# Performance work log

Hardware: AMD Instinct MI355X
Metric: run time of the kernel (lower is better)

Reference implementation:

```python
import jax, jax.numpy as jnp
import numpy as np

N_NODES = 100000
N_EDGES = 1600000
IN_F, HID, OUT_F = 256, 128, 48
ALPHA = 0.01
K = 10
# SparseDropout with dropout_prob=0 keeps all edges but scales by 1/(1-0+1e-5)
DROP_SCALE = 1.0 / (1.0 + 1e-5)


def setup_inputs() -> dict:
    key = jax.random.key(0)
    ks = jax.random.split(key, 8)
    x = jax.random.normal(ks[0], (N_NODES, IN_F), dtype=jnp.float32)
    rows = jax.random.randint(ks[1], (N_EDGES,), 0, N_NODES, dtype=jnp.int32)
    cols = jax.random.randint(ks[2], (N_EDGES,), 0, N_NODES, dtype=jnp.int32)
    vals = jax.random.uniform(ks[3], (N_EDGES,), dtype=jnp.float32)
    # Linear params (Kaiming-uniform-ish like torch defaults)
    lim1 = 1.0 / np.sqrt(IN_F)
    W1 = jax.random.uniform(ks[4], (IN_F, HID), minval=-lim1, maxval=lim1, dtype=jnp.float32)
    b1 = jax.random.uniform(ks[5], (HID,), minval=-lim1, maxval=lim1, dtype=jnp.float32)
    lim2 = 1.0 / np.sqrt(HID)
    W2 = jax.random.uniform(ks[6], (HID, OUT_F), minval=-lim2, maxval=lim2, dtype=jnp.float32)
    b2 = jax.random.uniform(ks[7], (OUT_F,), minval=-lim2, maxval=lim2, dtype=jnp.float32)
    return {"x": x, "rows": rows, "cols": cols, "vals": vals,
            "W1": W1, "b1": b1, "W2": W2, "b2": b2}


def reference(x, rows, cols, vals, W1, b1, W2, b2):
    # MLP (dropout=0 -> identity)
    h = jax.nn.relu(x @ W1 + b1)          # [N, HID]
    h = h @ W2 + b2                        # [N, OUT_F]
    v = vals * DROP_SCALE                  # SparseDropout(p=0) value scaling
    # K-step APPNP propagation: h <- (1-alpha) * A @ h + alpha * h
    def step(h, _):
        ah = jax.ops.segment_sum(v[:, None] * h[cols], rows, num_segments=N_NODES)
        return (1.0 - ALPHA) * ah + ALPHA * h, None
    h, _ = jax.lax.scan(step, h, None, length=K)
    return h
```

## Files before the change

kernel.cpp:

```cpp
#include <hip/hip_runtime.h>

#define N_NODES 100000
#define N_EDGES 1600000
#define IN_F 256
#define HID 128
#define OUT_F 48
#define PAD_F 64
#define ALPHA 0.01f
#define K_STEPS 10
#define DROP_SCALE (1.0f / (1.0f + 1e-5f))

#define NBUCK 196
#define BCAP 10240
#define EPB 4096
#define ROW_MASK_CLR 0xFFFFFFFFFC01FFFFULL

#define MLP_BLOCKS ((N_NODES / 16 + 3) / 4)
#define BUCKET_BLOCKS ((N_EDGES + EPB - 1) / EPB)

typedef __bf16 v8bf __attribute__((ext_vector_type(8)));
typedef float v4f __attribute__((ext_vector_type(4)));
typedef unsigned long long u64;

static __device__ __forceinline__ __bf16 tobf(float f) { return (__bf16)f; }

__global__ __launch_bounds__(256) void conv_w(const float* __restrict__ W1,
                                              const float* __restrict__ W2,
                                              __bf16* __restrict__ w1t,
                                              __bf16* __restrict__ w2t) {
  int i = blockIdx.x * 256 + threadIdx.x;
  if (i < HID * IN_F) {
    int n = i >> 8, k = i & 255;
    w1t[i] = tobf(W1[k * HID + n]);
  }
  int j = i - HID * IN_F;
  if (j >= 0 && j < OUT_F * HID) {
    int n = j >> 7, k = j & 127;
    w2t[j] = tobf(W2[k * OUT_F + n]);
  }
}

__global__ __launch_bounds__(256, 4) void fused_mlp_bucket(
    const float* __restrict__ x, const __bf16* __restrict__ w1t,
    const float* __restrict__ b1, const __bf16* __restrict__ w2t,
    const float* __restrict__ b2, __bf16* __restrict__ h0,
    const int* __restrict__ rows, const int* __restrict__ cols,
    const float* __restrict__ vals, int* __restrict__ bcur,
    u64* __restrict__ brec) {
  __shared__ __bf16 h1s[64][136];
  __shared__ int lhist[NBUCK];
  __shared__ int lbase[NBUCK];

  const int tid = threadIdx.x;

  if (blockIdx.x < MLP_BLOCKS) {
    const int wv = tid >> 6;
    const int l = tid & 63;
    const int lm = l & 15;
    const int ko = (l >> 4) * 8;
    const int gw = blockIdx.x * 4 + wv;
    if (gw >= N_NODES / 16) return;
    const int n0w = gw * 16;
    const int xrow = n0w + lm;

    const float* xb = x + (size_t)xrow * IN_F + ko;
    float4 xr[16];
#pragma unroll
    for (int k0 = 0; k0 < 8; k0++) {
      xr[2 * k0] = *(const float4*)(xb + k0 * 32);
      xr[2 * k0 + 1] = *(const float4*)(xb + k0 * 32 + 4);
    }

    v4f acc1[8];
#pragma unroll
    for (int nf = 0; nf < 8; nf++) acc1[nf] = (v4f){0.f, 0.f, 0.f, 0.f};

#pragma unroll
    for (int k0 = 0; k0 < 8; k0++) {
      const float* f0 = (const float*)&xr[2 * k0];
      v8bf a;
#pragma unroll
      for (int j = 0; j < 8; j++) a[j] = tobf(f0[j]);
      const __bf16* w1base = w1t + (size_t)lm * IN_F + k0 * 32 + ko;
#pragma unroll
      for (int nf = 0; nf < 8; nf++) {
        v8bf b = *(const v8bf*)(w1base + nf * 16 * IN_F);
        acc1[nf] = __builtin_amdgcn_mfma_f32_16x16x32_bf16(a, b, acc1[nf], 0, 0, 0);
      }
    }

#pragma unroll
    for (int nf = 0; nf < 8; nf++) {
      float bb = b1[nf * 16 + lm];
#pragma unroll
      for (int q = 0; q < 4; q++) {
        int rr = (wv << 4) + (l >> 4) * 4 + q;
        h1s[rr][nf * 16 + lm] = tobf(fmaxf(acc1[nf][q] + bb, 0.f));
      }
    }
    __syncthreads();

    const int lrow = (wv << 4) + lm;
    v4f acc2[3];
#pragma unroll
    for (int nf = 0; nf < 3; nf++) acc2[nf] = (v4f){0.f, 0.f, 0.f, 0.f};
    const __bf16* w2base = w2t + (size_t)lm * HID + ko;
#pragma unroll
    for (int k0 = 0; k0 < 4; k0++) {
      v8bf a = *(const v8bf*)&h1s[lrow][k0 * 32 + ko];
#pragma unroll
      for (int nf = 0; nf < 3; nf++) {
        v8bf b = *(const v8bf*)(w2base + nf * 16 * HID + k0 * 32);
        acc2[nf] = __builtin_amdgcn_mfma_f32_16x16x32_bf16(a, b, acc2[nf], 0, 0, 0);
      }
    }
#pragma unroll
    for (int nf = 0; nf < 3; nf++) {
      float bb = b2[nf * 16 + lm];
#pragma unroll
      for (int q = 0; q < 4; q++) {
        int node = n0w + (l >> 4) * 4 + q;
        h0[(size_t)node * PAD_F + nf * 16 + lm] = tobf(acc2[nf][q] + bb);
      }
    }
    if (l < 32) {
      uint4 z = make_uint4(0, 0, 0, 0);
      *(uint4*)(h0 + (size_t)(n0w + (l >> 1)) * PAD_F + 48 + (l & 1) * 8) = z;
    }
  } else {
    const int bid = blockIdx.x - MLP_BLOCKS;
    const int base = bid * EPB;

    for (int i = tid; i < NBUCK; i += 256) lhist[i] = 0;
    __syncthreads();

    u64 rec[16];
    short bb[16];
    short pp[16];
#pragma unroll
    for (int j = 0; j < 4; j++) {
      int e = base + j * 1024 + tid * 4;
      bool ok = e < N_EDGES;
      int4 r4 = ok ? *(const int4*)(rows + e) : make_int4(0, 0, 0, 0);
      int4 c4 = ok ? *(const int4*)(cols + e) : make_int4(0, 0, 0, 0);
      float4 v4 = ok ? *(const float4*)(vals + e) : make_float4(0, 0, 0, 0);
      int rr[4] = {r4.x, r4.y, r4.z, r4.w};
      int cc[4] = {c4.x, c4.y, c4.z, c4.w};
      float vv[4] = {v4.x, v4.y, v4.z, v4.w};
#pragma unroll
      for (int q = 0; q < 4; q++) {
        int idx = j * 4 + q;
        int b = rr[q] >> 9;
        float v = vv[q] * (DROP_SCALE * (1.0f - ALPHA));
        rec[idx] = ((u64)__float_as_uint(v) << 32) |
                   ((u64)(rr[q] & 511) << 17) | (unsigned)cc[q];
        bb[idx] = ok ? (short)b : (short)-1;
        pp[idx] = ok ? (short)atomicAdd(&lhist[b], 1) : (short)0;
      }
    }
    __syncthreads();

    for (int i = tid; i < NBUCK; i += 256) {
      int n = lhist[i];
      lbase[i] = (n > 0) ? atomicAdd(&bcur[i * 16], n) : 0;
    }
    __syncthreads();

#pragma unroll
    for (int j = 0; j < 16; j++) {
      if (bb[j] >= 0)
        brec[(size_t)bb[j] * BCAP + lbase[bb[j]] + pp[j]] = rec[j];
    }
  }
}

__global__ __launch_bounds__(256) void bscan_kernel(const int* __restrict__ bcur,
                                                    int* __restrict__ bstart,
                                                    int* __restrict__ rowptr) {
  __shared__ int s[256];
  int t = threadIdx.x;
  int v = (t < NBUCK) ? bcur[t * 16] : 0;
  s[t] = v;
  __syncthreads();
  for (int off = 1; off < 256; off <<= 1) {
    int add = (t >= off) ? s[t - off] : 0;
    __syncthreads();
    s[t] += add;
    __syncthreads();
  }
  if (t < NBUCK) bstart[t] = s[t] - v;
  if (t == 0) rowptr[N_NODES] = N_EDGES;
}

__global__ __launch_bounds__(512) void csr_kernel(
    const int* __restrict__ bcur, const int* __restrict__ bstart,
    const u64* __restrict__ brec, int* __restrict__ rowptr,
    u64* __restrict__ edges) {
  __shared__ int cnt[512];
  __shared__ int sc[512];
  const int b = blockIdx.x;
  const int t = threadIdx.x;
  const int n = bcur[b * 16];
  const int base = bstart[b];
  const size_t boff = (size_t)b * BCAP;

  cnt[t] = 0;
  __syncthreads();
  for (int i = t; i < n; i += 512)
    atomicAdd(&cnt[(int)((brec[boff + i] >> 17) & 511)], 1);
  __syncthreads();

  int v = cnt[t];
  sc[t] = v;
  __syncthreads();
  for (int off = 1; off < 512; off <<= 1) {
    int add = (t >= off) ? sc[t - off] : 0;
    __syncthreads();
    sc[t] += add;
    __syncthreads();
  }
  int excl = sc[t] - v;
  int grow = b * 512 + t;
  if (grow < N_NODES) rowptr[grow] = base + excl;
  cnt[t] = excl;
  __syncthreads();

  for (int i = t; i < n; i += 512) {
    u64 rec = brec[boff + i];
    int rr = (int)((rec >> 17) & 511);
    int p = atomicAdd(&cnt[rr], 1);
    edges[base + p] = rec & ROW_MASK_CLR;
  }
}

template <int FINAL>
__global__ __launch_bounds__(256) void prop_kernel(
    const __bf16* __restrict__ hin, __bf16* __restrict__ hout,
    float* __restrict__ fout, const int* __restrict__ rowptr,
    const u64* __restrict__ edges) {
  int wid = (blockIdx.x * 256 + threadIdx.x) >> 6;
  int lane = threadIdx.x & 63;
  if (wid >= N_NODES) return;
  const int g = lane >> 3;
  const int t = lane & 7;
  int s = __builtin_amdgcn_readfirstlane(rowptr[wid]);
  int e = __builtin_amdgcn_readfirstlane(rowptr[wid + 1]);

  float acc[8];
#pragma unroll
  for (int j = 0; j < 8; j++) acc[j] = 0.f;

  if (g == 0) {
    uint4 q = *(const uint4*)(hin + (size_t)wid * PAD_F + t * 8);
    unsigned uu[4] = {q.x, q.y, q.z, q.w};
#pragma unroll
    for (int k = 0; k < 4; k++) {
      acc[2 * k] = ALPHA * __uint_as_float(uu[k] << 16);
      acc[2 * k + 1] = ALPHA * __uint_as_float(uu[k] & 0xffff0000u);
    }
  }

  int i = s + g;
  for (; i + 8 < e; i += 16) {
    u64 r0 = edges[i];
    u64 r1 = edges[i + 8];
    int c0 = (int)(r0 & 0xffffffffu);
    int c1 = (int)(r1 & 0xffffffffu);
    float v0 = __uint_as_float((unsigned)(r0 >> 32));
    float v1 = __uint_as_float((unsigned)(r1 >> 32));
    uint4 q0 = *(const uint4*)(hin + (size_t)c0 * PAD_F + t * 8);
    uint4 q1 = *(const uint4*)(hin + (size_t)c1 * PAD_F + t * 8);
    unsigned a0[4] = {q0.x, q0.y, q0.z, q0.w};
    unsigned a1[4] = {q1.x, q1.y, q1.z, q1.w};
#pragma unroll
    for (int k = 0; k < 4; k++) {
      acc[2 * k] = fmaf(v0, __uint_as_float(a0[k] << 16), acc[2 * k]);
      acc[2 * k + 1] = fmaf(v0, __uint_as_float(a0[k] & 0xffff0000u), acc[2 * k + 1]);
    }
#pragma unroll
    for (int k = 0; k < 4; k++) {
      acc[2 * k] = fmaf(v1, __uint_as_float(a1[k] << 16), acc[2 * k]);
      acc[2 * k + 1] = fmaf(v1, __uint_as_float(a1[k] & 0xffff0000u), acc[2 * k + 1]);
    }
  }
  if (i < e) {
    u64 r0 = edges[i];
    int c0 = (int)(r0 & 0xffffffffu);
    float v0 = __uint_as_float((unsigned)(r0 >> 32));
    uint4 q0 = *(const uint4*)(hin + (size_t)c0 * PAD_F + t * 8);
    unsigned a0[4] = {q0.x, q0.y, q0.z, q0.w};
#pragma unroll
    for (int k = 0; k < 4; k++) {
      acc[2 * k] = fmaf(v0, __uint_as_float(a0[k] << 16), acc[2 * k]);
      acc[2 * k + 1] = fmaf(v0, __uint_as_float(a0[k] & 0xffff0000u), acc[2 * k + 1]);
    }
  }

#pragma unroll
  for (int m = 8; m <= 32; m <<= 1) {
#pragma unroll
    for (int j = 0; j < 8; j++) acc[j] += __shfl_xor(acc[j], m, 64);
  }

  if (g == 0) {
    if (FINAL) {
      if (t < 6) {
        float* dst = fout + (size_t)wid * OUT_F + t * 8;
        v4f lo4 = {acc[0], acc[1], acc[2], acc[3]};
        v4f hi4 = {acc[4], acc[5], acc[6], acc[7]};
        __builtin_nontemporal_store(lo4, (v4f*)dst);
        __builtin_nontemporal_store(hi4, (v4f*)(dst + 4));
      }
    } else {
      unsigned w[4];
#pragma unroll
      for (int k = 0; k < 4; k++) {
        unsigned short lo = __builtin_bit_cast(unsigned short, (__bf16)acc[2 * k]);
        unsigned short hi = __builtin_bit_cast(unsigned short, (__bf16)acc[2 * k + 1]);
        w[k] = ((unsigned)hi << 16) | lo;
      }
      *(uint4*)(hout + (size_t)wid * PAD_F + t * 8) =
          make_uint4(w[0], w[1], w[2], w[3]);
    }
  }
}

extern "C" void kernel_launch(void* const* d_in, const int* in_sizes, int n_in,
                              void* d_out, int out_size, void* d_ws,
                              size_t ws_size, hipStream_t stream) {
  const float* x = (const float*)d_in[0];
  const int* rows = (const int*)d_in[1];
  const int* cols = (const int*)d_in[2];
  const float* vals = (const float*)d_in[3];
  const float* W1 = (const float*)d_in[4];
  const float* b1 = (const float*)d_in[5];
  const float* W2 = (const float*)d_in[6];
  const float* b2 = (const float*)d_in[7];
  float* out = (float*)d_out;

  char* ws = (char*)d_ws;
  const size_t HA_OFF = 0;
  const size_t HB_OFF = 12800000;
  const size_t EDGES_OFF = 25600000;
  const size_t BREC_OFF = 38400000;
  const size_t ROWPTR_OFF = 54456320;
  const size_t BCUR_OFF = 54856448;
  const size_t BSTART_OFF = 54868992;
  const size_t W1T_OFF = 54870016;
  const size_t W2T_OFF = 54935552;

  __bf16* hA = (__bf16*)(ws + HA_OFF);
  __bf16* hB = (__bf16*)(ws + HB_OFF);
  u64* edges = (u64*)(ws + EDGES_OFF);
  u64* brec = (u64*)(ws + BREC_OFF);
  int* rowptr = (int*)(ws + ROWPTR_OFF);
  int* bcur = (int*)(ws + BCUR_OFF);
  int* bstart = (int*)(ws + BSTART_OFF);
  __bf16* w1t = (__bf16*)(ws + W1T_OFF);
  __bf16* w2t = (__bf16*)(ws + W2T_OFF);

  conv_w<<<(HID * IN_F + OUT_F * HID + 255) / 256, 256, 0, stream>>>(W1, W2,
                                                                     w1t, w2t);
  (void)hipMemsetAsync(bcur, 0, NBUCK * 64, stream);

  fused_mlp_bucket<<<MLP_BLOCKS + BUCKET_BLOCKS, 256, 0, stream>>>(
      x, w1t, b1, w2t, b2, hA, rows, cols, vals, bcur, brec);

  bscan_kernel<<<1, 256, 0, stream>>>(bcur, bstart, rowptr);
  csr_kernel<<<NBUCK, 512, 0, stream>>>(bcur, bstart, brec, rowptr, edges);

  const int PROP_BLOCKS = (N_NODES * 64 + 255) / 256;
  for (int k = 0; k < K_STEPS - 1; k++) {
    const __bf16* hin = (k & 1) ? hB : hA;
    __bf16* hout = (k & 1) ? hA : hB;
    prop_kernel<0><<<PROP_BLOCKS, 256, 0, stream>>>(hin, hout, nullptr, rowptr,
                                                    edges);
  }
  prop_kernel<1><<<PROP_BLOCKS, 256, 0, stream>>>(hB, nullptr, out, rowptr,
                                                  edges);
}
```

Baseline: 526.2 us.

## Remap SpMM propagation lanes to 4 edge groups × 16 feature lanes with 4x unroll

The propagation kernel now splits each wavefront into 4 edge groups of 16 lanes, each lane covering 4 bf16 features (8-byte loads), instead of 8 groups of 8 lanes with 16-byte loads. The main loop unrolls four edges per group, so 16 edge gathers are in flight per wave, and the cross-group reduction drops to two shuffles. A tail path handles leftover edges with a clamped index and a zero weight. A sched_barrier is also added in the MLP kernel after the x loads to keep them ahead of the MFMA loop. The per-lane gathers are narrower, which may lower memory efficiency.

```diff
diff --git a/kernel.cpp b/kernel.cpp
--- a/kernel.cpp
+++ b/kernel.cpp
@@ -70,6 +70,7 @@
       xr[2 * k0] = *(const float4*)(xb + k0 * 32);
       xr[2 * k0 + 1] = *(const float4*)(xb + k0 * 32 + 4);
     }
+    __builtin_amdgcn_sched_barrier(0);
 
     v4f acc1[8];
 #pragma unroll
@@ -241,86 +242,82 @@
   int wid = (blockIdx.x * 256 + threadIdx.x) >> 6;
   int lane = threadIdx.x & 63;
   if (wid >= N_NODES) return;
-  const int g = lane >> 3;
-  const int t = lane & 7;
+  const int eg = lane >> 4;
+  const int fq = lane & 15;
   int s = __builtin_amdgcn_readfirstlane(rowptr[wid]);
   int e = __builtin_amdgcn_readfirstlane(rowptr[wid + 1]);
 
-  float acc[8];
-#pragma unroll
-  for (int j = 0; j < 8; j++) acc[j] = 0.f;
-
-  if (g == 0) {
-    uint4 q = *(const uint4*)(hin + (size_t)wid * PAD_F + t * 8);
-    unsigned uu[4] = {q.x, q.y, q.z, q.w};
-#pragma unroll
-    for (int k = 0; k < 4; k++) {
-      acc[2 * k] = ALPHA * __uint_as_float(uu[k] << 16);
-      acc[2 * k + 1] = ALPHA * __uint_as_float(uu[k] & 0xffff0000u);
-    }
-  }
-
-  int i = s + g;
-  for (; i + 8 < e; i += 16) {
-    u64 r0 = edges[i];
-    u64 r1 = edges[i + 8];
-    int c0 = (int)(r0 & 0xffffffffu);
-    int c1 = (int)(r1 & 0xffffffffu);
-    float v0 = __uint_as_float((unsigned)(r0 >> 32));
-    float v1 = __uint_as_float((unsigned)(r1 >> 32));
-    uint4 q0 = *(const uint4*)(hin + (size_t)c0 * PAD_F + t * 8);
-    uint4 q1 = *(const uint4*)(hin + (size_t)c1 * PAD_F + t * 8);
-    unsigned a0[4] = {q0.x, q0.y, q0.z, q0.w};
-    unsigned a1[4] = {q1.x, q1.y, q1.z, q1.w};
-#pragma unroll
-    for (int k = 0; k < 4; k++) {
-      acc[2 * k] = fmaf(v0, __uint_as_float(a0[k] << 16), acc[2 * k]);
-      acc[2 * k + 1] = fmaf(v0, __uint_as_float(a0[k] & 0xffff0000u), acc[2 * k + 1]);
-    }
-#pragma unroll
-    for (int k = 0; k < 4; k++) {
-      acc[2 * k] = fmaf(v1, __uint_as_float(a1[k] << 16), acc[2 * k]);
-      acc[2 * k + 1] = fmaf(v1, __uint_as_float(a1[k] & 0xffff0000u), acc[2 * k + 1]);
-    }
+  float acc[4] = {0.f, 0.f, 0.f, 0.f};
+  if (eg == 0) {
+    uint2 q = *(const uint2*)(hin + (size_t)wid * PAD_F + fq * 4);
+    acc[0] = ALPHA * __uint_as_float(q.x << 16);
+    acc[1] = ALPHA * __uint_as_float(q.x & 0xffff0000u);
+    acc[2] = ALPHA * __uint_as_float(q.y << 16);
+    acc[3] = ALPHA * __uint_as_float(q.y & 0xffff0000u);
+  }
+
+  int i = s;
+  for (; i + 16 <= e; i += 16) {
+    u64 r[4];
+#pragma unroll
+    for (int u = 0; u < 4; u++) r[u] = edges[i + u * 4 + eg];
+    uint2 q[4];
+#pragma unroll
+    for (int u = 0; u < 4; u++)
+      q[u] = *(const uint2*)(hin + (size_t)(unsigned)(r[u] & 0xffffffffu) * PAD_F +
+                             fq * 4);
+#pragma unroll
+    for (int u = 0; u < 4; u++) {
+      float v = __uint_as_float((unsigned)(r[u] >> 32));
+      acc[0] = fmaf(v, __uint_as_float(q[u].x << 16), acc[0]);
+      acc[1] = fmaf(v, __uint_as_float(q[u].x & 0xffff0000u), acc[1]);
+      acc[2] = fmaf(v, __uint_as_float(q[u].y << 16), acc[2]);
+      acc[3] = fmaf(v, __uint_as_float(q[u].y & 0xffff0000u), acc[3]);
+    }
+  }
+  for (; i + 4 <= e; i += 4) {
+    u64 r = edges[i + eg];
+    uint2 q = *(const uint2*)(hin + (size_t)(unsigned)(r & 0xffffffffu) * PAD_F +
+                              fq * 4);
+    float v = __uint_as_float((unsigned)(r >> 32));
+    acc[0] = fmaf(v, __uint_as_float(q.x << 16), acc[0]);
+    acc[1] = fmaf(v, __uint_as_float(q.x & 0xffff0000u), acc[1]);
+    acc[2] = fmaf(v, __uint_as_float(q.y << 16), acc[2]);
+    acc[3] = fmaf(v, __uint_as_float(q.y & 0xffff0000u), acc[3]);
   }
   if (i < e) {
-    u64 r0 = edges[i];
-    int c0 = (int)(r0 & 0xffffffffu);
-    float v0 = __uint_as_float((unsigned)(r0 >> 32));
-    uint4 q0 = *(const uint4*)(hin + (size_t)c0 * PAD_F + t * 8);
-    unsigned a0[4] = {q0.x, q0.y, q0.z, q0.w};
-#pragma unroll
-    for (int k = 0; k < 4; k++) {
-      acc[2 * k] = fmaf(v0, __uint_as_float(a0[k] << 16), acc[2 * k]);
-      acc[2 * k + 1] = fmaf(v0, __uint_as_float(a0[k] & 0xffff0000u), acc[2 * k + 1]);
-    }
-  }
-
-#pragma unroll
-  for (int m = 8; m <= 32; m <<= 1) {
-#pragma unroll
-    for (int j = 0; j < 8; j++) acc[j] += __shfl_xor(acc[j], m, 64);
-  }
-
-  if (g == 0) {
+    int idx = i + eg;
+    u64 r = edges[idx < e ? idx : (e - 1)];
+    uint2 q = *(const uint2*)(hin + (size_t)(unsigned)(r & 0xffffffffu) * PAD_F +
+                              fq * 4);
+    float v = (idx < e) ? __uint_as_float((unsigned)(r >> 32)) : 0.f;
+    acc[0] = fmaf(v, __uint_as_float(q.x << 16), acc[0]);
+    acc[1] = fmaf(v, __uint_as_float(q.x & 0xffff0000u), acc[1]);
+    acc[2] = fmaf(v, __uint_as_float(q.y << 16), acc[2]);
+    acc[3] = fmaf(v, __uint_as_float(q.y & 0xffff0000u), acc[3]);
+  }
+
+#pragma unroll
+  for (int j = 0; j < 4; j++) {
+    acc[j] += __shfl_xor(acc[j], 16, 64);
+    acc[j] += __shfl_xor(acc[j], 32, 64);
+  }
+
+  if (eg == 0) {
     if (FINAL) {
-      if (t < 6) {
-        float* dst = fout + (size_t)wid * OUT_F + t * 8;
-        v4f lo4 = {acc[0], acc[1], acc[2], acc[3]};
-        v4f hi4 = {acc[4], acc[5], acc[6], acc[7]};
-        __builtin_nontemporal_store(lo4, (v4f*)dst);
-        __builtin_nontemporal_store(hi4, (v4f*)(dst + 4));
+      if (fq < 12) {
+        v4f o = {acc[0], acc[1], acc[2], acc[3]};
+        __builtin_nontemporal_store(o, (v4f*)(fout + (size_t)wid * OUT_F + fq * 4));
       }
     } else {
-      unsigned w[4];
-#pragma unroll
-      for (int k = 0; k < 4; k++) {
-        unsigned short lo = __builtin_bit_cast(unsigned short, (__bf16)acc[2 * k]);
-        unsigned short hi = __builtin_bit_cast(unsigned short, (__bf16)acc[2 * k + 1]);
-        w[k] = ((unsigned)hi << 16) | lo;
-      }
-      *(uint4*)(hout + (size_t)wid * PAD_F + t * 8) =
-          make_uint4(w[0], w[1], w[2], w[3]);
+      unsigned short b0 = __builtin_bit_cast(unsigned short, (__bf16)acc[0]);
+      unsigned short b1 = __builtin_bit_cast(unsigned short, (__bf16)acc[1]);
+      unsigned short b2 = __builtin_bit_cast(unsigned short, (__bf16)acc[2]);
+      unsigned short b3 = __builtin_bit_cast(unsigned short, (__bf16)acc[3]);
+      uint2 w;
+      w.x = ((unsigned)b1 << 16) | b0;
+      w.y = ((unsigned)b3 << 16) | b2;
+      *(uint2*)(hout + (size_t)wid * PAD_F + fq * 4) = w;
     }
   }
 }
```

After: 598.7 us. +13.8%, slower.

## Split MLP from bucketing and pre-convert x to bf16 in a fused prep kernel

Applied to the files above, without the earlier changes.

Moves the x fp32-to-bf16 conversion and the weight transpose into a single prep kernel that also does edge bucketing. The MLP then runs as a separate MFMA kernel reading bf16 x. This is meant to shrink the MLP's register load and improve its load efficiency. In exchange it adds an extra write and read of the full bf16 copy of x, plus one more kernel launch. The workspace layout is rearranged so xb aliases hB.

```diff
diff --git a/kernel.cpp b/kernel.cpp
--- a/kernel.cpp
+++ b/kernel.cpp
@@ -15,120 +15,56 @@
 #define EPB 4096
 #define ROW_MASK_CLR 0xFFFFFFFFFC01FFFFULL
 
-#define MLP_BLOCKS ((N_NODES / 16 + 3) / 4)
-#define BUCKET_BLOCKS ((N_EDGES + EPB - 1) / EPB)
+#define XCONV_BLOCKS 6250
+#define CONVW_BLOCKS 153
+#define BUCKET_BLOCKS 391
 
 typedef __bf16 v8bf __attribute__((ext_vector_type(8)));
 typedef float v4f __attribute__((ext_vector_type(4)));
 typedef unsigned long long u64;
 
 static __device__ __forceinline__ __bf16 tobf(float f) { return (__bf16)f; }
-
-__global__ __launch_bounds__(256) void conv_w(const float* __restrict__ W1,
-                                              const float* __restrict__ W2,
-                                              __bf16* __restrict__ w1t,
-                                              __bf16* __restrict__ w2t) {
-  int i = blockIdx.x * 256 + threadIdx.x;
-  if (i < HID * IN_F) {
-    int n = i >> 8, k = i & 255;
-    w1t[i] = tobf(W1[k * HID + n]);
-  }
-  int j = i - HID * IN_F;
-  if (j >= 0 && j < OUT_F * HID) {
-    int n = j >> 7, k = j & 127;
-    w2t[j] = tobf(W2[k * OUT_F + n]);
-  }
-}
-
-__global__ __launch_bounds__(256, 4) void fused_mlp_bucket(
-    const float* __restrict__ x, const __bf16* __restrict__ w1t,
-    const float* __restrict__ b1, const __bf16* __restrict__ w2t,
-    const float* __restrict__ b2, __bf16* __restrict__ h0,
+static __device__ __forceinline__ unsigned pack2(float a, float b) {
+  unsigned short lo = __builtin_bit_cast(unsigned short, (__bf16)a);
+  unsigned short hi = __builtin_bit_cast(unsigned short, (__bf16)b);
+  return ((unsigned)hi << 16) | lo;
+}
+
+__global__ __launch_bounds__(256) void fused_pre(
+    const float* __restrict__ x, const float* __restrict__ W1,
+    const float* __restrict__ W2, __bf16* __restrict__ xb,
+    __bf16* __restrict__ w1t, __bf16* __restrict__ w2t,
     const int* __restrict__ rows, const int* __restrict__ cols,
     const float* __restrict__ vals, int* __restrict__ bcur,
     u64* __restrict__ brec) {
-  __shared__ __bf16 h1s[64][136];
   __shared__ int lhist[NBUCK];
   __shared__ int lbase[NBUCK];
-
   const int tid = threadIdx.x;
 
-  if (blockIdx.x < MLP_BLOCKS) {
-    const int wv = tid >> 6;
-    const int l = tid & 63;
-    const int lm = l & 15;
-    const int ko = (l >> 4) * 8;
-    const int gw = blockIdx.x * 4 + wv;
-    if (gw >= N_NODES / 16) return;
-    const int n0w = gw * 16;
-    const int xrow = n0w + lm;
-
-    const float* xb = x + (size_t)xrow * IN_F + ko;
-    float4 xr[16];
-#pragma unroll
-    for (int k0 = 0; k0 < 8; k0++) {
-      xr[2 * k0] = *(const float4*)(xb + k0 * 32);
-      xr[2 * k0 + 1] = *(const float4*)(xb + k0 * 32 + 4);
-    }
-
-    v4f acc1[8];
-#pragma unroll
-    for (int nf = 0; nf < 8; nf++) acc1[nf] = (v4f){0.f, 0.f, 0.f, 0.f};
-
-#pragma unroll
-    for (int k0 = 0; k0 < 8; k0++) {
-      const float* f0 = (const float*)&xr[2 * k0];
-      v8bf a;
-#pragma unroll
-      for (int j = 0; j < 8; j++) a[j] = tobf(f0[j]);
-      const __bf16* w1base = w1t + (size_t)lm * IN_F + k0 * 32 + ko;
-#pragma unroll
-      for (int nf = 0; nf < 8; nf++) {
-        v8bf b = *(const v8bf*)(w1base + nf * 16 * IN_F);
-        acc1[nf] = __builtin_amdgcn_mfma_f32_16x16x32_bf16(a, b, acc1[nf], 0, 0, 0);
-      }
-    }
-
-#pragma unroll
-    for (int nf = 0; nf < 8; nf++) {
-      float bb = b1[nf * 16 + lm];
-#pragma unroll
-      for (int q = 0; q < 4; q++) {
-        int rr = (wv << 4) + (l >> 4) * 4 + q;
-        h1s[rr][nf * 16 + lm] = tobf(fmaxf(acc1[nf][q] + bb, 0.f));
-      }
-    }
-    __syncthreads();
-
-    const int lrow = (wv << 4) + lm;
-    v4f acc2[3];
-#pragma unroll
-    for (int nf = 0; nf < 3; nf++) acc2[nf] = (v4f){0.f, 0.f, 0.f, 0.f};
-    const __bf16* w2base = w2t + (size_t)lm * HID + ko;
-#pragma unroll
-    for (int k0 = 0; k0 < 4; k0++) {
-      v8bf a = *(const v8bf*)&h1s[lrow][k0 * 32 + ko];
-#pragma unroll
-      for (int nf = 0; nf < 3; nf++) {
-        v8bf b = *(const v8bf*)(w2base + nf * 16 * HID + k0 * 32);
-        acc2[nf] = __builtin_amdgcn_mfma_f32_16x16x32_bf16(a, b, acc2[nf], 0, 0, 0);
-      }
-    }
-#pragma unroll
-    for (int nf = 0; nf < 3; nf++) {
-      float bb = b2[nf * 16 + lm];
-#pragma unroll
-      for (int q = 0; q < 4; q++) {
-        int node = n0w + (l >> 4) * 4 + q;
-        h0[(size_t)node * PAD_F + nf * 16 + lm] = tobf(acc2[nf][q] + bb);
-      }
-    }
-    if (l < 32) {
-      uint4 z = make_uint4(0, 0, 0, 0);
-      *(uint4*)(h0 + (size_t)(n0w + (l >> 1)) * PAD_F + 48 + (l & 1) * 8) = z;
+  if (blockIdx.x < XCONV_BLOCKS) {
+    int c = blockIdx.x * 256 + tid;
+    const float4* xp = (const float4*)(x + (size_t)c * 16);
+    float4 f0 = xp[0], f1 = xp[1], f2 = xp[2], f3 = xp[3];
+    uint4 o0 = make_uint4(pack2(f0.x, f0.y), pack2(f0.z, f0.w),
+                          pack2(f1.x, f1.y), pack2(f1.z, f1.w));
+    uint4 o1 = make_uint4(pack2(f2.x, f2.y), pack2(f2.z, f2.w),
+                          pack2(f3.x, f3.y), pack2(f3.z, f3.w));
+    uint4* op = (uint4*)(xb + (size_t)c * 16);
+    op[0] = o0;
+    op[1] = o1;
+  } else if (blockIdx.x < XCONV_BLOCKS + CONVW_BLOCKS) {
+    int i = (blockIdx.x - XCONV_BLOCKS) * 256 + tid;
+    if (i < HID * IN_F) {
+      int n = i >> 8, k = i & 255;
+      w1t[i] = tobf(W1[k * HID + n]);
+    }
+    int j = i - HID * IN_F;
+    if (j >= 0 && j < OUT_F * HID) {
+      int n = j >> 7, k = j & 127;
+      w2t[j] = tobf(W2[k * OUT_F + n]);
     }
   } else {
-    const int bid = blockIdx.x - MLP_BLOCKS;
+    const int bid = blockIdx.x - XCONV_BLOCKS - CONVW_BLOCKS;
     const int base = bid * EPB;
 
     for (int i = tid; i < NBUCK; i += 256) lhist[i] = 0;
@@ -171,6 +107,81 @@
       if (bb[j] >= 0)
         brec[(size_t)bb[j] * BCAP + lbase[bb[j]] + pp[j]] = rec[j];
     }
+  }
+}
+
+__global__ __launch_bounds__(256, 4) void mlp_mfma(
+    const __bf16* __restrict__ xb, const __bf16* __restrict__ w1t,
+    const float* __restrict__ b1, const __bf16* __restrict__ w2t,
+    const float* __restrict__ b2, __bf16* __restrict__ h0) {
+  __shared__ __bf16 h1s[64][136];
+
+  const int tid = threadIdx.x;
+  const int wv = tid >> 6;
+  const int l = tid & 63;
+  const int lm = l & 15;
+  const int ko = (l >> 4) * 8;
+  const int gw = blockIdx.x * 4 + wv;
+  if (gw >= N_NODES / 16) return;
+  const int n0w = gw * 16;
+  const int xrow = n0w + lm;
+
+  const __bf16* xbr = xb + (size_t)xrow * IN_F + ko;
+  v8bf a8[8];
+#pragma unroll
+  for (int k0 = 0; k0 < 8; k0++) a8[k0] = *(const v8bf*)(xbr + k0 * 32);
+
+  v4f acc1[8];
+#pragma unroll
+  for (int nf = 0; nf < 8; nf++) acc1[nf] = (v4f){0.f, 0.f, 0.f, 0.f};
+
+#pragma unroll
+  for (int k0 = 0; k0 < 8; k0++) {
+    const __bf16* w1base = w1t + (size_t)lm * IN_F + k0 * 32 + ko;
+#pragma unroll
+    for (int nf = 0; nf < 8; nf++) {
+      v8bf b = *(const v8bf*)(w1base + nf * 16 * IN_F);
+      acc1[nf] = __builtin_amdgcn_mfma_f32_16x16x32_bf16(a8[k0], b, acc1[nf], 0, 0, 0);
+    }
+  }
+
+#pragma unroll
+  for (int nf = 0; nf < 8; nf++) {
+    float bb = b1[nf * 16 + lm];
+#pragma unroll
+    for (int q = 0; q < 4; q++) {
+      int rr = (wv << 4) + (l >> 4) * 4 + q;
+      h1s[rr][nf * 16 + lm] = tobf(fmaxf(acc1[nf][q] + bb, 0.f));
+    }
+  }
+  __syncthreads();
+
+  const int lrow = (wv << 4) + lm;
+  v4f acc2[3];
+#pragma unroll
+  for (int nf = 0; nf < 3; nf++) acc2[nf] = (v4f){0.f, 0.f, 0.f, 0.f};
+  const __bf16* w2base = w2t + (size_t)lm * HID + ko;
+#pragma unroll
+  for (int k0 = 0; k0 < 4; k0++) {
+    v8bf a = *(const v8bf*)&h1s[lrow][k0 * 32 + ko];
+#pragma unroll
+    for (int nf = 0; nf < 3; nf++) {
+      v8bf b = *(const v8bf*)(w2base + nf * 16 * HID + k0 * 32);
+      acc2[nf] = __builtin_amdgcn_mfma_f32_16x16x32_bf16(a, b, acc2[nf], 0, 0, 0);
+    }
+  }
+#pragma unroll
+  for (int nf = 0; nf < 3; nf++) {
+    float bb = b2[nf * 16 + lm];
+#pragma unroll
+    for (int q = 0; q < 4; q++) {
+      int node = n0w + (l >> 4) * 4 + q;
+      h0[(size_t)node * PAD_F + nf * 16 + lm] = tobf(acc2[nf][q] + bb);
+    }
+  }
+  if (l < 32) {
+    uint4 z = make_uint4(0, 0, 0, 0);
+    *(uint4*)(h0 + (size_t)(n0w + (l >> 1)) * PAD_F + 48 + (l & 1) * 8) = z;
   }
 }
 
@@ -339,16 +350,18 @@
   float* out = (float*)d_out;
 
   char* ws = (char*)d_ws;
-  const size_t HA_OFF = 0;
-  const size_t HB_OFF = 12800000;
-  const size_t EDGES_OFF = 25600000;
-  const size_t BREC_OFF = 38400000;
-  const size_t ROWPTR_OFF = 54456320;
-  const size_t BCUR_OFF = 54856448;
-  const size_t BSTART_OFF = 54868992;
-  const size_t W1T_OFF = 54870016;
-  const size_t W2T_OFF = 54935552;
-
+  const size_t XB_OFF = 0;
+  const size_t HB_OFF = 0;
+  const size_t EDGES_OFF = 12800000;
+  const size_t HA_OFF = 51200000;
+  const size_t BREC_OFF = 64000000;
+  const size_t ROWPTR_OFF = 80056320;
+  const size_t BCUR_OFF = 80456448;
+  const size_t BSTART_OFF = 80469248;
+  const size_t W1T_OFF = 80470272;
+  const size_t W2T_OFF = 80535808;
+
+  __bf16* xb = (__bf16*)(ws + XB_OFF);
   __bf16* hA = (__bf16*)(ws + HA_OFF);
   __bf16* hB = (__bf16*)(ws + HB_OFF);
   u64* edges = (u64*)(ws + EDGES_OFF);
@@ -359,12 +372,12 @@
   __bf16* w1t = (__bf16*)(ws + W1T_OFF);
   __bf16* w2t = (__bf16*)(ws + W2T_OFF);
 
-  conv_w<<<(HID * IN_F + OUT_F * HID + 255) / 256, 256, 0, stream>>>(W1, W2,
-                                                                     w1t, w2t);
   (void)hipMemsetAsync(bcur, 0, NBUCK * 64, stream);
 
-  fused_mlp_bucket<<<MLP_BLOCKS + BUCKET_BLOCKS, 256, 0, stream>>>(
-      x, w1t, b1, w2t, b2, hA, rows, cols, vals, bcur, brec);
+  fused_pre<<<XCONV_BLOCKS + CONVW_BLOCKS + BUCKET_BLOCKS, 256, 0, stream>>>(
+      x, W1, W2, xb, w1t, w2t, rows, cols, vals, bcur, brec);
+
+  mlp_mfma<<<(N_NODES / 16 + 3) / 4, 256, 0, stream>>>(xb, w1t, b1, w2t, b2, hA);
 
   bscan_kernel<<<1, 256, 0, stream>>>(bcur, bstart, rowptr);
   csr_kernel<<<NBUCK, 512, 0, stream>>>(bcur, bstart, brec, rowptr, edges);
```

Measured after the change: 550.4 us. 1.05x slower.
